# Optimization experiments

Hardware: AMD Instinct MI355X
Metric: run time of the kernel (lower is better)

Reference implementation:

```python
import jax, jax.numpy as jnp
import numpy as np

B, T, C, H, M = 2, 2048, 1024, 16, 64
EPS = 1e-5


def _ln(x, g, b):
    mu = jnp.mean(x, axis=-1, keepdims=True)
    var = jnp.mean(jnp.square(x - mu), axis=-1, keepdims=True)
    return (x - mu) * jax.lax.rsqrt(var + EPS) * g + b


def setup_inputs() -> dict:
    key = jax.random.key(0)
    ks = jax.random.split(key, 16)
    s = lambda fan_in: 1.0 / np.sqrt(fan_in)
    return {
        'x': jax.random.normal(ks[0], (B, T, C), jnp.float32),
        'ln1_g': jnp.ones((C,), jnp.float32),
        'ln1_b': jnp.zeros((C,), jnp.float32),
        'attn_w': jax.random.normal(ks[1], (C, 3 * C), jnp.float32) * s(C),
        'attn_b': jnp.zeros((3 * C,), jnp.float32),
        'proj_w': jax.random.normal(ks[2], (C, C), jnp.float32) * s(C),
        'proj_b': jnp.zeros((C,), jnp.float32),
        'a1_dw': jax.random.normal(ks[3], (C, M), jnp.float32) * s(C),
        'a1_db': jnp.zeros((M,), jnp.float32),
        'a1_uw': jax.random.normal(ks[4], (M, C), jnp.float32) * s(M),
        'a1_ub': jnp.zeros((C,), jnp.float32),
        'ln2_g': jnp.ones((C,), jnp.float32),
        'ln2_b': jnp.zeros((C,), jnp.float32),
        'fc_w': jax.random.normal(ks[5], (C, 4 * C), jnp.float32) * s(C),
        'fc_b': jnp.zeros((4 * C,), jnp.float32),
        'mlp_pw': jax.random.normal(ks[6], (4 * C, C), jnp.float32) * s(4 * C),
        'mlp_pb': jnp.zeros((C,), jnp.float32),
        'a2_dw': jax.random.normal(ks[7], (C, M), jnp.float32) * s(C),
        'a2_db': jnp.zeros((M,), jnp.float32),
        'a2_uw': jax.random.normal(ks[8], (M, C), jnp.float32) * s(M),
        'a2_ub': jnp.zeros((C,), jnp.float32),
    }


def _attn(x, attn_w, attn_b, proj_w, proj_b):
    b, t, c = x.shape
    hd = c // H
    qkv = x @ attn_w + attn_b                      # [B,T,3C]
    q, k, v = jnp.split(qkv, 3, axis=-1)
    q = q.reshape(b, t, H, hd).transpose(0, 2, 1, 3)  # [B,H,T,hd]
    k = k.reshape(b, t, H, hd).transpose(0, 2, 1, 3)
    v = v.reshape(b, t, H, hd).transpose(0, 2, 1, 3)
    att = jnp.einsum('bhqd,bhkd->bhqk', q, k) * (1.0 / np.sqrt(hd))
    mask = jnp.tril(jnp.ones((t, t), bool))
    att = jnp.where(mask, att, -jnp.inf)
    att = jax.nn.softmax(att, axis=-1)
    y = jnp.einsum('bhqk,bhkd->bhqd', att, v)      # [B,H,T,hd]
    y = y.transpose(0, 2, 1, 3).reshape(b, t, c)
    return y @ proj_w + proj_b


def _adapter(x, dw, db, uw, ub):
    return jax.nn.relu(x @ dw + db) @ uw + ub


def reference(x, ln1_g, ln1_b, attn_w, attn_b, proj_w, proj_b,
              a1_dw, a1_db, a1_uw, a1_ub, ln2_g, ln2_b,
              fc_w, fc_b, mlp_pw, mlp_pb, a2_dw, a2_db, a2_uw, a2_ub):
    x = x + _attn(_ln(x, ln1_g, ln1_b), attn_w, attn_b, proj_w, proj_b)
    x = x + _adapter(x, a1_dw, a1_db, a1_uw, a1_ub)
    h = _ln(x, ln2_g, ln2_b)
    h = jax.nn.gelu(h @ fc_w + fc_b, approximate=True) @ mlp_pw + mlp_pb
    x = x + h
    x = x + _adapter(x, a2_dw, a2_db, a2_uw, a2_ub)
    return x
```

## Files before the change

kernel.cpp:

```cpp
#include <hip/hip_runtime.h>
#include <hip/hip_bf16.h>
#include <cstdint>

#define DEVI __device__ __forceinline__

using bf16x8 = __attribute__((ext_vector_type(8))) short;
using f32x4  = __attribute__((ext_vector_type(4))) float;

DEVI short f2b(float f) {
  __hip_bfloat16 h = __float2bfloat16(f);
  return *reinterpret_cast<short*>(&h);
}

DEVI f32x4 mfma16(bf16x8 a, bf16x8 b, f32x4 c) {
  return __builtin_amdgcn_mfma_f32_16x16x32_bf16(a, b, c, 0, 0, 0);
}

DEVI void gload_lds16(const void* g, void* l) {
  __builtin_amdgcn_global_load_lds(
      (const __attribute__((address_space(1))) void*)g,
      (__attribute__((address_space(3))) void*)l, 16, 0, 0);
}

DEVI float gelu_f(float x) {
  float u = 1.5957691216057308f * (x + 0.044715f * x * x * x);
  float e = __expf(u);
  float t = 1.f - 2.f / (e + 1.f);
  return 0.5f * x * (1.f + t);
}

__global__ void k_wt(const float* __restrict__ in, short* __restrict__ out,
                     int R, int Cc) {
  __shared__ float tile[32][33];
  int c0 = blockIdx.x * 32;
  int r0 = blockIdx.y * 32;
  int tx = threadIdx.x, ty = threadIdx.y;
  for (int i = ty; i < 32; i += 8) {
    int r = r0 + i, c = c0 + tx;
    tile[i][tx] = (r < R && c < Cc) ? in[(size_t)r * Cc + c] : 0.f;
  }
  __syncthreads();
  for (int i = ty; i < 32; i += 8) {
    int orow = c0 + i;
    int ocol = r0 + tx;
    if (orow < Cc && ocol < R) out[(size_t)orow * R + ocol] = f2b(tile[tx][i]);
  }
}

__global__ void k_layernorm(const float* __restrict__ x, const float* __restrict__ g,
                            const float* __restrict__ bta, short* __restrict__ out) {
  const int C = 1024;
  int row = blockIdx.x;
  const float* xr = x + (size_t)row * C;
  f32x4 v = *(const f32x4*)(xr + threadIdx.x * 4);
  float s = v[0] + v[1] + v[2] + v[3];
  float s2 = v[0]*v[0] + v[1]*v[1] + v[2]*v[2] + v[3]*v[3];
#pragma unroll
  for (int m = 1; m < 64; m <<= 1) { s += __shfl_xor(s, m); s2 += __shfl_xor(s2, m); }
  __shared__ float red[8];
  int w = threadIdx.x >> 6;
  if ((threadIdx.x & 63) == 0) { red[w] = s; red[4 + w] = s2; }
  __syncthreads();
  s = red[0] + red[1] + red[2] + red[3];
  s2 = red[4] + red[5] + red[6] + red[7];
  float mu = s * (1.f / 1024.f);
  float rstd = rsqrtf(s2 * (1.f / 1024.f) - mu * mu + 1e-5f);
#pragma unroll
  for (int j = 0; j < 4; ++j) {
    int c = threadIdx.x * 4 + j;
    out[(size_t)row * C + c] = f2b((v[j] - mu) * rstd * g[c] + bta[c]);
  }
}

__global__ void k_vtrans(const short* __restrict__ qkv, short* __restrict__ vT) {
  __shared__ short tile[32][72];
  int b = blockIdx.z, h = blockIdx.y;
  int t0 = blockIdx.x * 32;
  int tx = threadIdx.x;
  int ty = threadIdx.y;
  const size_t inbase = ((size_t)(b * 2048 + t0)) * 3072 + 2048 + h * 64;
  for (int i = ty; i < 32; i += 8) {
    tile[i][tx]      = qkv[inbase + (size_t)i * 3072 + tx];
    tile[i][tx + 32] = qkv[inbase + (size_t)i * 3072 + tx + 32];
  }
  __syncthreads();
  const size_t outbase = ((size_t)(b * 16 + h) * 64) * 2048 + t0;
  for (int d = ty; d < 64; d += 8)
    vT[outbase + (size_t)d * 2048 + tx] = tile[tx][d];
}

template <int BM, int BN, int WGM, int WGN, int ACT, bool RESID, bool OUTF, bool OUTB>
__global__ __launch_bounds__(256, 2) void k_gemm(
    const short* __restrict__ A, const short* __restrict__ BT,
    const float* __restrict__ bias, const float* __restrict__ resid,
    float* __restrict__ outf, short* __restrict__ outb,
    int M, int N, int K) {
  static_assert(WGM * WGN == 4, "4 waves");
  constexpr int TM = BM / WGM, TN = BN / WGN;
  constexpr int FM = TM / 16, FN = TN / 16;
  __shared__ short As[BM * 32];
  __shared__ short Bs[BN * 32];
  const int tid = threadIdx.x;
  const int wid = tid >> 6, l = tid & 63, lr = l & 15, lg = l >> 4;
  const int wm = wid / WGN, wn = wid % WGN;
  const int rowA0 = blockIdx.x * BM;
  const int colB0 = blockIdx.y * BN;

  f32x4 acc[FM][FN];
#pragma unroll
  for (int i = 0; i < FM; ++i)
#pragma unroll
    for (int j = 0; j < FN; ++j) acc[i][j] = f32x4{0.f, 0.f, 0.f, 0.f};

  for (int k0 = 0; k0 < K; k0 += 32) {
    __syncthreads();
#pragma unroll
    for (int it = 0; it < (BM * 64) / 4096; ++it) {
      int bo = it * 4096 + tid * 16;
      int row = bo >> 6, col = (bo & 63) >> 1;
      gload_lds16(A + (size_t)(rowA0 + row) * K + k0 + col, (void*)(As + (bo >> 1)));
    }
#pragma unroll
    for (int it = 0; it < (BN * 64) / 4096; ++it) {
      int bo = it * 4096 + tid * 16;
      int row = bo >> 6, col = (bo & 63) >> 1;
      gload_lds16(BT + (size_t)(colB0 + row) * K + k0 + col, (void*)(Bs + (bo >> 1)));
    }
    __syncthreads();
    bf16x8 af[FM], bfr[FN];
#pragma unroll
    for (int i = 0; i < FM; ++i)
      af[i] = *(const bf16x8*)(As + (wm * TM + i * 16 + lr) * 32 + lg * 8);
#pragma unroll
    for (int j = 0; j < FN; ++j)
      bfr[j] = *(const bf16x8*)(Bs + (wn * TN + j * 16 + lr) * 32 + lg * 8);
#pragma unroll
    for (int i = 0; i < FM; ++i)
#pragma unroll
      for (int j = 0; j < FN; ++j)
        acc[i][j] = mfma16(af[i], bfr[j], acc[i][j]);
  }

  const int row0 = rowA0 + wm * TM + lg * 4;
  const int col0 = colB0 + wn * TN + lr;
#pragma unroll
  for (int i = 0; i < FM; ++i) {
#pragma unroll
    for (int j = 0; j < FN; ++j) {
#pragma unroll
      for (int r = 0; r < 4; ++r) {
        int row = row0 + i * 16 + r;
        int col = col0 + j * 16;
        float v = acc[i][j][r] + bias[col];
        if (ACT == 1) v = fmaxf(v, 0.f);
        if (ACT == 2) v = gelu_f(v);
        size_t idx = (size_t)row * N + col;
        if (RESID) v += resid[idx];
        if (OUTF) outf[idx] = v;
        if (OUTB) outb[idx] = f2b(v);
      }
    }
  }
}

__global__ __launch_bounds__(256, 2) void k_attn(
    const short* __restrict__ qkv, const short* __restrict__ vT,
    short* __restrict__ y) {
  constexpr int T = 2048, C3 = 3072;
  const int tid = threadIdx.x;
  const int wid = tid >> 6, l = tid & 63, lr = l & 15, lg = l >> 4;
  const int bh = blockIdx.x, b = bh >> 4, h = bh & 15;
  const int q0 = blockIdx.y * 64 + wid * 16;

  __shared__ short Plds[4][16][32];

  const short* qptr = qkv + (size_t)(b * T + q0) * C3 + h * 64;
  bf16x8 qf0 = *(const bf16x8*)(qptr + (size_t)lr * C3 + lg * 8);
  bf16x8 qf1 = *(const bf16x8*)(qptr + (size_t)lr * C3 + 32 + lg * 8);

  const short* kbase = qkv + (size_t)(b * T) * C3 + 1024 + h * 64;
  const short* vtb = vT + (size_t)bh * 64 * 2048;

  f32x4 o[4];
#pragma unroll
  for (int d = 0; d < 4; ++d) o[d] = f32x4{0.f, 0.f, 0.f, 0.f};
  float mrow[4] = {-1e30f, -1e30f, -1e30f, -1e30f};
  float lsum[4] = {0.f, 0.f, 0.f, 0.f};

  const int kvend = q0 + 16;
  for (int kv0 = 0; kv0 < kvend; kv0 += 32) {
    bf16x8 kf00 = *(const bf16x8*)(kbase + (size_t)(kv0 + lr) * C3 + lg * 8);
    bf16x8 kf01 = *(const bf16x8*)(kbase + (size_t)(kv0 + lr) * C3 + 32 + lg * 8);
    bf16x8 kf10 = *(const bf16x8*)(kbase + (size_t)(kv0 + 16 + lr) * C3 + lg * 8);
    bf16x8 kf11 = *(const bf16x8*)(kbase + (size_t)(kv0 + 16 + lr) * C3 + 32 + lg * 8);
    f32x4 s0 = {0.f, 0.f, 0.f, 0.f}, s1 = {0.f, 0.f, 0.f, 0.f};
    s0 = mfma16(qf0, kf00, s0);
    s0 = mfma16(qf1, kf01, s0);
    s1 = mfma16(qf0, kf10, s1);
    s1 = mfma16(qf1, kf11, s1);
#pragma unroll
    for (int r = 0; r < 4; ++r) {
      const int qrow = q0 + lg * 4 + r;
      float v0 = s0[r] * 0.125f;
      float v1 = s1[r] * 0.125f;
      if (kv0 + lr > qrow) v0 = -1e30f;
      if (kv0 + 16 + lr > qrow) v1 = -1e30f;
      float mt = fmaxf(v0, v1);
      mt = fmaxf(mt, __shfl_xor(mt, 1));
      mt = fmaxf(mt, __shfl_xor(mt, 2));
      mt = fmaxf(mt, __shfl_xor(mt, 4));
      mt = fmaxf(mt, __shfl_xor(mt, 8));
      float mnew = fmaxf(mrow[r], mt);
      float corr = __expf(mrow[r] - mnew);
      mrow[r] = mnew;
      float p0 = __expf(v0 - mnew);
      float p1 = __expf(v1 - mnew);
      lsum[r] = lsum[r] * corr + p0 + p1;
      o[0][r] *= corr; o[1][r] *= corr; o[2][r] *= corr; o[3][r] *= corr;
      Plds[wid][lg * 4 + r][lr] = f2b(p0);
      Plds[wid][lg * 4 + r][16 + lr] = f2b(p1);
    }
    bf16x8 pf = *(const bf16x8*)(&Plds[wid][lr][lg * 8]);
#pragma unroll
    for (int db = 0; db < 4; ++db) {
      bf16x8 vf = *(const bf16x8*)(vtb + (size_t)(db * 16 + lr) * 2048 + kv0 + lg * 8);
      o[db] = mfma16(pf, vf, o[db]);
    }
  }
  float inv[4];
#pragma unroll
  for (int r = 0; r < 4; ++r) {
    float s = lsum[r];
    s += __shfl_xor(s, 1); s += __shfl_xor(s, 2);
    s += __shfl_xor(s, 4); s += __shfl_xor(s, 8);
    inv[r] = 1.f / s;
  }
#pragma unroll
  for (int db = 0; db < 4; ++db)
#pragma unroll
    for (int r = 0; r < 4; ++r)
      y[(size_t)(b * T + q0 + lg * 4 + r) * 1024 + h * 64 + db * 16 + lr] =
          f2b(o[db][r] * inv[r]);
}

extern "C" void kernel_launch(void* const* d_in, const int* in_sizes, int n_in,
                              void* d_out, int out_size, void* d_ws, size_t ws_size,
                              hipStream_t stream) {
  (void)in_sizes; (void)n_in; (void)out_size; (void)ws_size;
  const float* x0     = (const float*)d_in[0];
  const float* ln1_g  = (const float*)d_in[1];
  const float* ln1_b  = (const float*)d_in[2];
  const float* attn_w = (const float*)d_in[3];
  const float* attn_b = (const float*)d_in[4];
  const float* proj_w = (const float*)d_in[5];
  const float* proj_b = (const float*)d_in[6];
  const float* a1_dw  = (const float*)d_in[7];
  const float* a1_db  = (const float*)d_in[8];
  const float* a1_uw  = (const float*)d_in[9];
  const float* a1_ub  = (const float*)d_in[10];
  const float* ln2_g  = (const float*)d_in[11];
  const float* ln2_b  = (const float*)d_in[12];
  const float* fc_w   = (const float*)d_in[13];
  const float* fc_b   = (const float*)d_in[14];
  const float* mlp_pw = (const float*)d_in[15];
  const float* mlp_pb = (const float*)d_in[16];
  const float* a2_dw  = (const float*)d_in[17];
  const float* a2_db  = (const float*)d_in[18];
  const float* a2_uw  = (const float*)d_in[19];
  const float* a2_ub  = (const float*)d_in[20];

  char* ws = (char*)d_ws;
  size_t off = 0;
  auto alloc = [&](size_t bytes) {
    char* p = ws + off;
    off = (off + bytes + 255) & ~(size_t)255;
    return p;
  };

  short* attn_wT = (short*)alloc(3072ull * 1024 * 2);
  short* proj_wT = (short*)alloc(1024ull * 1024 * 2);
  short* fc_wT   = (short*)alloc(4096ull * 1024 * 2);
  short* mlp_pwT = (short*)alloc(1024ull * 4096 * 2);
  short* a1_dwT  = (short*)alloc(64ull * 1024 * 2);
  short* a1_uwT  = (short*)alloc(1024ull * 64 * 2);
  short* a2_dwT  = (short*)alloc(64ull * 1024 * 2);
  short* a2_uwT  = (short*)alloc(1024ull * 64 * 2);
  short* lnb     = (short*)alloc(4096ull * 1024 * 2);
  char*  big     = alloc(4096ull * 4096 * 2);
  short* qkvb    = (short*)big;
  short* vTb     = (short*)(big + 4096ull * 3072 * 2);
  short* fcb     = (short*)big;
  short* yb      = (short*)alloc(4096ull * 1024 * 2);
  float* x1f     = (float*)alloc(4096ull * 1024 * 4);
  float* x2f     = (float*)alloc(4096ull * 1024 * 4);
  short* x1b     = (short*)alloc(4096ull * 1024 * 2);
  short* hb      = (short*)alloc(4096ull * 64 * 2);

  dim3 tb(32, 8);
  k_wt<<<dim3(3072 / 32, 1024 / 32), tb, 0, stream>>>(attn_w, attn_wT, 1024, 3072);
  k_wt<<<dim3(1024 / 32, 1024 / 32), tb, 0, stream>>>(proj_w, proj_wT, 1024, 1024);
  k_wt<<<dim3(4096 / 32, 1024 / 32), tb, 0, stream>>>(fc_w, fc_wT, 1024, 4096);
  k_wt<<<dim3(1024 / 32, 4096 / 32), tb, 0, stream>>>(mlp_pw, mlp_pwT, 4096, 1024);
  k_wt<<<dim3(64 / 32, 1024 / 32), tb, 0, stream>>>(a1_dw, a1_dwT, 1024, 64);
  k_wt<<<dim3(1024 / 32, 64 / 32), tb, 0, stream>>>(a1_uw, a1_uwT, 64, 1024);
  k_wt<<<dim3(64 / 32, 1024 / 32), tb, 0, stream>>>(a2_dw, a2_dwT, 1024, 64);
  k_wt<<<dim3(1024 / 32, 64 / 32), tb, 0, stream>>>(a2_uw, a2_uwT, 64, 1024);

  k_layernorm<<<4096, 256, 0, stream>>>(x0, ln1_g, ln1_b, lnb);

  k_gemm<128, 128, 2, 2, 0, false, false, true><<<dim3(32, 24), 256, 0, stream>>>(
      lnb, attn_wT, attn_b, nullptr, nullptr, qkvb, 4096, 3072, 1024);

  k_vtrans<<<dim3(64, 16, 2), tb, 0, stream>>>(qkvb, vTb);

  k_attn<<<dim3(32, 32), 256, 0, stream>>>(qkvb, vTb, yb);

  k_gemm<128, 128, 2, 2, 0, true, true, true><<<dim3(32, 8), 256, 0, stream>>>(
      yb, proj_wT, proj_b, x0, x1f, x1b, 4096, 1024, 1024);

  k_gemm<128, 64, 4, 1, 1, false, false, true><<<dim3(32, 1), 256, 0, stream>>>(
      x1b, a1_dwT, a1_db, nullptr, nullptr, hb, 4096, 64, 1024);

  k_gemm<128, 128, 2, 2, 0, true, true, false><<<dim3(32, 8), 256, 0, stream>>>(
      hb, a1_uwT, a1_ub, x1f, x2f, nullptr, 4096, 1024, 64);

  k_layernorm<<<4096, 256, 0, stream>>>(x2f, ln2_g, ln2_b, lnb);

  k_gemm<128, 128, 2, 2, 2, false, false, true><<<dim3(32, 32), 256, 0, stream>>>(
      lnb, fc_wT, fc_b, nullptr, nullptr, fcb, 4096, 4096, 1024);

  k_gemm<128, 128, 2, 2, 0, true, true, true><<<dim3(32, 8), 256, 0, stream>>>(
      fcb, mlp_pwT, mlp_pb, x2f, x1f, x1b, 4096, 1024, 4096);

  k_gemm<128, 64, 4, 1, 1, false, false, true><<<dim3(32, 1), 256, 0, stream>>>(
      x1b, a2_dwT, a2_db, nullptr, nullptr, hb, 4096, 64, 1024);

  k_gemm<128, 128, 2, 2, 0, true, true, false><<<dim3(32, 8), 256, 0, stream>>>(
      hb, a2_uwT, a2_ub, x1f, (float*)d_out, nullptr, 4096, 1024, 64);
}
```

Measured before the change: 556.1 us.

## Restructure attention: transposed MFMA, exp2 softmax with lazy rescale, reverse tile order

The attention kernel now computes S^T so each lane owns one query row. That removes the per-row cross-lane max and sum shuffles, and the output is written as packed 4-element stores. Q is prescaled by log2(e)/8 so exp2 can be used. The running max is only updated when it grows by more than 8, and masking is applied only on the final diagonal tile. Query tiles run in reverse order so the longer causal blocks start first, launch bounds allow four blocks per CU, and the adapter down-projection GEMM uses smaller 64x64 tiles to get more blocks. The risks are bf16 rounding of the scaled Q and extra register pressure under the higher occupancy target.

```diff
diff --git a/kernel.cpp b/kernel.cpp
--- a/kernel.cpp
+++ b/kernel.cpp
@@ -10,6 +10,13 @@
 DEVI short f2b(float f) {
   __hip_bfloat16 h = __float2bfloat16(f);
   return *reinterpret_cast<short*>(&h);
+}
+DEVI float b2f(short s) {
+  __hip_bfloat16 h = *reinterpret_cast<__hip_bfloat16*>(&s);
+  return __bfloat162float(h);
+}
+DEVI uint32_t pk2(float a, float b) {
+  return (uint32_t)(uint16_t)f2b(a) | ((uint32_t)(uint16_t)f2b(b) << 16);
 }
 
 DEVI f32x4 mfma16(bf16x8 a, bf16x8 b, f32x4 c) {
@@ -163,20 +170,28 @@
   }
 }
 
-__global__ __launch_bounds__(256, 2) void k_attn(
+__global__ __launch_bounds__(256, 4) void k_attn(
     const short* __restrict__ qkv, const short* __restrict__ vT,
     short* __restrict__ y) {
   constexpr int T = 2048, C3 = 3072;
   const int tid = threadIdx.x;
   const int wid = tid >> 6, l = tid & 63, lr = l & 15, lg = l >> 4;
   const int bh = blockIdx.x, b = bh >> 4, h = bh & 15;
-  const int q0 = blockIdx.y * 64 + wid * 16;
+  const int qt = (int)(gridDim.y - 1 - blockIdx.y);
+  const int q0 = qt * 64 + wid * 16;
 
   __shared__ short Plds[4][16][32];
 
-  const short* qptr = qkv + (size_t)(b * T + q0) * C3 + h * 64;
-  bf16x8 qf0 = *(const bf16x8*)(qptr + (size_t)lr * C3 + lg * 8);
-  bf16x8 qf1 = *(const bf16x8*)(qptr + (size_t)lr * C3 + 32 + lg * 8);
+  const float qscale = 0.125f * 1.4426950408889634f;
+  const short* qptr = qkv + (size_t)(b * T + q0 + lr) * C3 + h * 64;
+  bf16x8 qr0 = *(const bf16x8*)(qptr + lg * 8);
+  bf16x8 qr1 = *(const bf16x8*)(qptr + 32 + lg * 8);
+  bf16x8 qf0, qf1;
+#pragma unroll
+  for (int j = 0; j < 8; ++j) {
+    qf0[j] = f2b(b2f(qr0[j]) * qscale);
+    qf1[j] = f2b(b2f(qr1[j]) * qscale);
+  }
 
   const short* kbase = qkv + (size_t)(b * T) * C3 + 1024 + h * 64;
   const short* vtb = vT + (size_t)bh * 64 * 2048;
@@ -184,63 +199,77 @@
   f32x4 o[4];
 #pragma unroll
   for (int d = 0; d < 4; ++d) o[d] = f32x4{0.f, 0.f, 0.f, 0.f};
-  float mrow[4] = {-1e30f, -1e30f, -1e30f, -1e30f};
-  float lsum[4] = {0.f, 0.f, 0.f, 0.f};
-
-  const int kvend = q0 + 16;
-  for (int kv0 = 0; kv0 < kvend; kv0 += 32) {
-    bf16x8 kf00 = *(const bf16x8*)(kbase + (size_t)(kv0 + lr) * C3 + lg * 8);
-    bf16x8 kf01 = *(const bf16x8*)(kbase + (size_t)(kv0 + lr) * C3 + 32 + lg * 8);
-    bf16x8 kf10 = *(const bf16x8*)(kbase + (size_t)(kv0 + 16 + lr) * C3 + lg * 8);
-    bf16x8 kf11 = *(const bf16x8*)(kbase + (size_t)(kv0 + 16 + lr) * C3 + 32 + lg * 8);
+  float m = -1e30f, lsum = 0.f;
+
+  const int kv_full = q0 & ~31;
+
+  auto body = [&](int kv0, bool mask) {
+    const short* kp = kbase + (size_t)(kv0 + lr) * C3;
+    bf16x8 kf00 = *(const bf16x8*)(kp + lg * 8);
+    bf16x8 kf01 = *(const bf16x8*)(kp + 32 + lg * 8);
+    const short* kp1 = kp + (size_t)16 * C3;
+    bf16x8 kf10 = *(const bf16x8*)(kp1 + lg * 8);
+    bf16x8 kf11 = *(const bf16x8*)(kp1 + 32 + lg * 8);
     f32x4 s0 = {0.f, 0.f, 0.f, 0.f}, s1 = {0.f, 0.f, 0.f, 0.f};
-    s0 = mfma16(qf0, kf00, s0);
-    s0 = mfma16(qf1, kf01, s0);
-    s1 = mfma16(qf0, kf10, s1);
-    s1 = mfma16(qf1, kf11, s1);
-#pragma unroll
-    for (int r = 0; r < 4; ++r) {
-      const int qrow = q0 + lg * 4 + r;
-      float v0 = s0[r] * 0.125f;
-      float v1 = s1[r] * 0.125f;
-      if (kv0 + lr > qrow) v0 = -1e30f;
-      if (kv0 + 16 + lr > qrow) v1 = -1e30f;
-      float mt = fmaxf(v0, v1);
-      mt = fmaxf(mt, __shfl_xor(mt, 1));
-      mt = fmaxf(mt, __shfl_xor(mt, 2));
-      mt = fmaxf(mt, __shfl_xor(mt, 4));
-      mt = fmaxf(mt, __shfl_xor(mt, 8));
-      float mnew = fmaxf(mrow[r], mt);
-      float corr = __expf(mrow[r] - mnew);
-      mrow[r] = mnew;
-      float p0 = __expf(v0 - mnew);
-      float p1 = __expf(v1 - mnew);
-      lsum[r] = lsum[r] * corr + p0 + p1;
-      o[0][r] *= corr; o[1][r] *= corr; o[2][r] *= corr; o[3][r] *= corr;
-      Plds[wid][lg * 4 + r][lr] = f2b(p0);
-      Plds[wid][lg * 4 + r][16 + lr] = f2b(p1);
-    }
-    bf16x8 pf = *(const bf16x8*)(&Plds[wid][lr][lg * 8]);
-#pragma unroll
-    for (int db = 0; db < 4; ++db) {
-      bf16x8 vf = *(const bf16x8*)(vtb + (size_t)(db * 16 + lr) * 2048 + kv0 + lg * 8);
-      o[db] = mfma16(pf, vf, o[db]);
-    }
-  }
-  float inv[4];
-#pragma unroll
-  for (int r = 0; r < 4; ++r) {
-    float s = lsum[r];
-    s += __shfl_xor(s, 1); s += __shfl_xor(s, 2);
-    s += __shfl_xor(s, 4); s += __shfl_xor(s, 8);
-    inv[r] = 1.f / s;
-  }
-#pragma unroll
-  for (int db = 0; db < 4; ++db)
-#pragma unroll
-    for (int r = 0; r < 4; ++r)
-      y[(size_t)(b * T + q0 + lg * 4 + r) * 1024 + h * 64 + db * 16 + lr] =
-          f2b(o[db][r] * inv[r]);
+    s0 = mfma16(kf00, qf0, s0);
+    s0 = mfma16(kf01, qf1, s0);
+    s1 = mfma16(kf10, qf0, s1);
+    s1 = mfma16(kf11, qf1, s1);
+    if (mask) {
+      const int q = q0 + lr;
+#pragma unroll
+      for (int r = 0; r < 4; ++r) {
+        if (kv0 + lg * 4 + r > q) s0[r] = -1e30f;
+        if (kv0 + 16 + lg * 4 + r > q) s1[r] = -1e30f;
+      }
+    }
+    float mx = fmaxf(fmaxf(fmaxf(s0[0], s0[1]), fmaxf(s0[2], s0[3])),
+                     fmaxf(fmaxf(s1[0], s1[1]), fmaxf(s1[2], s1[3])));
+    mx = fmaxf(mx, __shfl_xor(mx, 16));
+    mx = fmaxf(mx, __shfl_xor(mx, 32));
+    if (__any(mx > m + 8.f)) {
+      float mn = fmaxf(m, mx);
+      float corr = exp2f(m - mn);
+      m = mn;
+      lsum *= corr;
+#pragma unroll
+      for (int d = 0; d < 4; ++d)
+#pragma unroll
+        for (int r = 0; r < 4; ++r) o[d][r] *= corr;
+    }
+    float p0 = exp2f(s0[0] - m), p1 = exp2f(s0[1] - m);
+    float p2 = exp2f(s0[2] - m), p3 = exp2f(s0[3] - m);
+    float p4 = exp2f(s1[0] - m), p5 = exp2f(s1[1] - m);
+    float p6 = exp2f(s1[2] - m), p7 = exp2f(s1[3] - m);
+    lsum += ((p0 + p1) + (p2 + p3)) + ((p4 + p5) + (p6 + p7));
+    uint2 w0, w1;
+    w0.x = pk2(p0, p1); w0.y = pk2(p2, p3);
+    w1.x = pk2(p4, p5); w1.y = pk2(p6, p7);
+    *(uint2*)&Plds[wid][lr][lg * 4] = w0;
+    *(uint2*)&Plds[wid][lr][16 + lg * 4] = w1;
+    bf16x8 pf = *(const bf16x8*)&Plds[wid][lr][lg * 8];
+#pragma unroll
+    for (int dt = 0; dt < 4; ++dt) {
+      bf16x8 vf = *(const bf16x8*)(vtb + (size_t)(dt * 16 + lr) * 2048 + kv0 + lg * 8);
+      o[dt] = mfma16(vf, pf, o[dt]);
+    }
+  };
+
+  for (int kv0 = 0; kv0 < kv_full; kv0 += 32) body(kv0, false);
+  body(kv_full, true);
+
+  lsum += __shfl_xor(lsum, 16);
+  lsum += __shfl_xor(lsum, 32);
+  float inv = 1.f / lsum;
+
+  short* yp = y + (size_t)(b * T + q0 + lr) * 1024 + h * 64;
+#pragma unroll
+  for (int dt = 0; dt < 4; ++dt) {
+    uint2 wv;
+    wv.x = pk2(o[dt][0] * inv, o[dt][1] * inv);
+    wv.y = pk2(o[dt][2] * inv, o[dt][3] * inv);
+    *(uint2*)(yp + dt * 16 + lg * 4) = wv;
+  }
 }
 
 extern "C" void kernel_launch(void* const* d_in, const int* in_sizes, int n_in,
@@ -318,7 +347,7 @@
   k_gemm<128, 128, 2, 2, 0, true, true, true><<<dim3(32, 8), 256, 0, stream>>>(
       yb, proj_wT, proj_b, x0, x1f, x1b, 4096, 1024, 1024);
 
-  k_gemm<128, 64, 4, 1, 1, false, false, true><<<dim3(32, 1), 256, 0, stream>>>(
+  k_gemm<64, 64, 2, 2, 1, false, false, true><<<dim3(64, 1), 256, 0, stream>>>(
       x1b, a1_dwT, a1_db, nullptr, nullptr, hb, 4096, 64, 1024);
 
   k_gemm<128, 128, 2, 2, 0, true, true, false><<<dim3(32, 8), 256, 0, stream>>>(
@@ -332,7 +361,7 @@
   k_gemm<128, 128, 2, 2, 0, true, true, true><<<dim3(32, 8), 256, 0, stream>>>(
       fcb, mlp_pwT, mlp_pb, x2f, x1f, x1b, 4096, 1024, 4096);
 
-  k_gemm<128, 64, 4, 1, 1, false, false, true><<<dim3(32, 1), 256, 0, stream>>>(
+  k_gemm<64, 64, 2, 2, 1, false, false, true><<<dim3(64, 1), 256, 0, stream>>>(
       x1b, a2_dwT, a2_db, nullptr, nullptr, hb, 4096, 64, 1024);
 
   k_gemm<128, 128, 2, 2, 0, true, true, false><<<dim3(32, 8), 256, 0, stream>>>(
```

Result: no change. 559.6 us (+0.6%).
